# Kernel tuning notes

Measured on AMD Instinct MI355X. Metric: run time of the kernel, lower is better.

## Reference

```python
import jax, jax.numpy as jnp
import numpy as np

NUM_HEADS = 8
HEAD_DIM = 64  # inner_dim 512 / 8 heads
SCALE = HEAD_DIM ** -0.5


def setup_inputs() -> dict:
    key = jax.random.key(0)
    kq, kk, kv, kp = jax.random.split(key, 4)
    B, S, D = 8, 1024, 512
    q = jax.random.normal(kq, (B, S, D), dtype=jnp.float32)
    k = jax.random.normal(kk, (B, S, D), dtype=jnp.float32)
    v = jax.random.normal(kv, (B, S, D), dtype=jnp.float32)
    # learned additive positional bias table (trunc-normal init approximated by normal clipped)
    pos_bias = jnp.clip(jax.random.normal(kp, (1, NUM_HEADS, S, S), dtype=jnp.float32), -2.0, 2.0)
    return {"q": q, "k": k, "v": v, "pos_bias": pos_bias}


def reference(q, k, v, pos_bias):
    B, S, D = q.shape
    h, d = NUM_HEADS, HEAD_DIM
    # b n (h d) -> b h n d
    qh = q.reshape(B, S, h, d).transpose(0, 2, 1, 3) * SCALE
    kh = k.reshape(B, S, h, d).transpose(0, 2, 1, 3)
    vh = v.reshape(B, S, h, d).transpose(0, 2, 1, 3)
    sim = jnp.einsum('bhid,bhjd->bhij', qh, kh) + pos_bias
    attn = jax.nn.softmax(sim, axis=-1)
    out = jnp.einsum('bhij,bhjd->bhid', attn, vh)
    # b h n d -> b n (h d)
    return out.transpose(0, 2, 1, 3).reshape(B, S, h * d)
```

## Files before the change

### kernel.cpp

```cpp
#include <hip/hip_runtime.h>
#include <hip/hip_bf16.h>
#include <math.h>


typedef __attribute__((ext_vector_type(8))) short short8;
typedef __attribute__((ext_vector_type(4))) float f32x4;
typedef __attribute__((ext_vector_type(4))) unsigned short u16x4;

#define SEQ   1024
#define DM    512
#define HD    64
#define SCALE 0.125f

__device__ __forceinline__ unsigned short f2bf(float f) {
    unsigned u = __float_as_uint(f);
    u += 0x7fffu + ((u >> 16) & 1u);
    return (unsigned short)(u >> 16);
}

__device__ __forceinline__ u16x4 pack4(float a, float b, float c, float d) {
    u16x4 r; r[0] = f2bf(a); r[1] = f2bf(b); r[2] = f2bf(c); r[3] = f2bf(d);
    return r;
}

__global__ __launch_bounds__(256, 3)
void attn_fwd(const float* __restrict__ q, const float* __restrict__ k,
              const float* __restrict__ v, const float* __restrict__ bias,
              float* __restrict__ out)
{
    __shared__ short Klds[64][72];
    __shared__ short Vt[64][72];
    __shared__ short Plds[4][16][72];

    const int t    = threadIdx.x;
    const int wid  = t >> 6;
    const int lane = t & 63;
    const int qr   = lane & 15;
    const int g    = lane >> 4;

    int idx = blockIdx.x;
    const int b = idx & 7;  idx >>= 3;
    const int h = idx & 7;
    const int qtile = idx >> 3;
    const int qbase = qtile * 64 + wid * 16;

    const float* qp = q + ((b * SEQ + qbase + qr) * DM + h * HD);
    short8 qf[2];
#pragma unroll
    for (int c = 0; c < 2; ++c) {
        float4 x0 = *reinterpret_cast<const float4*>(qp + g * 8 + 32 * c);
        float4 x1 = *reinterpret_cast<const float4*>(qp + g * 8 + 32 * c + 4);
        short8 f;
        f[0] = (short)f2bf(x0.x * SCALE); f[1] = (short)f2bf(x0.y * SCALE);
        f[2] = (short)f2bf(x0.z * SCALE); f[3] = (short)f2bf(x0.w * SCALE);
        f[4] = (short)f2bf(x1.x * SCALE); f[5] = (short)f2bf(x1.y * SCALE);
        f[6] = (short)f2bf(x1.z * SCALE); f[7] = (short)f2bf(x1.w * SCALE);
        qf[c] = f;
    }

    f32x4 o[4];
#pragma unroll
    for (int nt = 0; nt < 4; ++nt) o[nt] = (f32x4){0.f, 0.f, 0.f, 0.f};
    float mrun = -INFINITY, lrun = 0.f;

    const int jrow = t & 63;
    const int cc   = t >> 6;

    for (int kt = 0; kt < 16; ++kt) {
        const int kbase = kt * 64;

        {
            const float4* kp4 = reinterpret_cast<const float4*>(
                k + ((b * SEQ + kbase + jrow) * DM + h * HD + cc * 16));
            float4 a0 = kp4[0], a1 = kp4[1], a2 = kp4[2], a3 = kp4[3];
            u16x4* dst = reinterpret_cast<u16x4*>(&Klds[jrow][cc * 16]);
            dst[0] = pack4(a0.x, a0.y, a0.z, a0.w);
            dst[1] = pack4(a1.x, a1.y, a1.z, a1.w);
            dst[2] = pack4(a2.x, a2.y, a2.z, a2.w);
            dst[3] = pack4(a3.x, a3.y, a3.z, a3.w);
        }
        {
            const float* vp = v + ((b * SEQ + kbase + cc * 16) * DM + h * HD + jrow);
            float vv[16];
#pragma unroll
            for (int jj = 0; jj < 16; ++jj) vv[jj] = vp[jj * DM];
            u16x4* dst = reinterpret_cast<u16x4*>(&Vt[jrow][cc * 16]);
            dst[0] = pack4(vv[0],  vv[1],  vv[2],  vv[3]);
            dst[1] = pack4(vv[4],  vv[5],  vv[6],  vv[7]);
            dst[2] = pack4(vv[8],  vv[9],  vv[10], vv[11]);
            dst[3] = pack4(vv[12], vv[13], vv[14], vv[15]);
        }
        __syncthreads();

        const float* bp = bias + ((h * SEQ + qbase + qr) * SEQ + kbase + g * 4);
        float4 bv0 = *reinterpret_cast<const float4*>(bp);
        float4 bv1 = *reinterpret_cast<const float4*>(bp + 16);
        float4 bv2 = *reinterpret_cast<const float4*>(bp + 32);
        float4 bv3 = *reinterpret_cast<const float4*>(bp + 48);

        f32x4 acc[4];
#pragma unroll
        for (int mt = 0; mt < 4; ++mt) {
            f32x4 a = (f32x4){0.f, 0.f, 0.f, 0.f};
#pragma unroll
            for (int c = 0; c < 2; ++c) {
                short8 kf = *reinterpret_cast<const short8*>(
                    &Klds[qr + 16 * mt][g * 8 + 32 * c]);
                a = __builtin_amdgcn_mfma_f32_16x16x32_bf16(kf, qf[c], a, 0, 0, 0);
            }
            acc[mt] = a;
        }
        acc[0][0] += bv0.x; acc[0][1] += bv0.y; acc[0][2] += bv0.z; acc[0][3] += bv0.w;
        acc[1][0] += bv1.x; acc[1][1] += bv1.y; acc[1][2] += bv1.z; acc[1][3] += bv1.w;
        acc[2][0] += bv2.x; acc[2][1] += bv2.y; acc[2][2] += bv2.z; acc[2][3] += bv2.w;
        acc[3][0] += bv3.x; acc[3][1] += bv3.y; acc[3][2] += bv3.z; acc[3][3] += bv3.w;

        float tmax = acc[0][0];
#pragma unroll
        for (int mt = 0; mt < 4; ++mt)
#pragma unroll
            for (int r = 0; r < 4; ++r) tmax = fmaxf(tmax, acc[mt][r]);
        tmax = fmaxf(tmax, __shfl_xor(tmax, 16));
        tmax = fmaxf(tmax, __shfl_xor(tmax, 32));
        const float mnew = fmaxf(mrun, tmax);

        float p[4][4];
        float ssum = 0.f;
#pragma unroll
        for (int mt = 0; mt < 4; ++mt)
#pragma unroll
            for (int r = 0; r < 4; ++r) {
                float e = __expf(acc[mt][r] - mnew);
                p[mt][r] = e;
                ssum += e;
            }
        ssum += __shfl_xor(ssum, 16);
        ssum += __shfl_xor(ssum, 32);
        const float sc = __expf(mrun - mnew);
        lrun = lrun * sc + ssum;
        mrun = mnew;

#pragma unroll
        for (int mt = 0; mt < 4; ++mt) {
            *reinterpret_cast<u16x4*>(&Plds[wid][qr][16 * mt + g * 4]) =
                pack4(p[mt][0], p[mt][1], p[mt][2], p[mt][3]);
        }

        float scr[4];
#pragma unroll
        for (int r = 0; r < 4; ++r) scr[r] = __shfl(sc, g * 4 + r);
#pragma unroll
        for (int nt = 0; nt < 4; ++nt)
#pragma unroll
            for (int r = 0; r < 4; ++r) o[nt][r] *= scr[r];

        asm volatile("s_waitcnt lgkmcnt(0)" ::: "memory");

        short8 pf0 = *reinterpret_cast<const short8*>(&Plds[wid][qr][g * 8]);
        short8 pf1 = *reinterpret_cast<const short8*>(&Plds[wid][qr][g * 8 + 32]);
#pragma unroll
        for (int nt = 0; nt < 4; ++nt) {
            short8 vf0 = *reinterpret_cast<const short8*>(&Vt[qr + 16 * nt][g * 8]);
            short8 vf1 = *reinterpret_cast<const short8*>(&Vt[qr + 16 * nt][g * 8 + 32]);
            o[nt] = __builtin_amdgcn_mfma_f32_16x16x32_bf16(pf0, vf0, o[nt], 0, 0, 0);
            o[nt] = __builtin_amdgcn_mfma_f32_16x16x32_bf16(pf1, vf1, o[nt], 0, 0, 0);
        }
        __syncthreads();
    }

    const float inv = 1.0f / lrun;
    float invr[4];
#pragma unroll
    for (int r = 0; r < 4; ++r) invr[r] = __shfl(inv, g * 4 + r);

    float* op = out + ((b * SEQ + qbase) * DM + h * HD + qr);
#pragma unroll
    for (int nt = 0; nt < 4; ++nt)
#pragma unroll
        for (int r = 0; r < 4; ++r)
            op[(g * 4 + r) * DM + nt * 16] = o[nt][r] * invr[r];
}

extern "C" void kernel_launch(void* const* d_in, const int* in_sizes, int n_in,
                              void* d_out, int out_size, void* d_ws, size_t ws_size,
                              hipStream_t stream) {
    const float* q    = (const float*)d_in[0];
    const float* k    = (const float*)d_in[1];
    const float* v    = (const float*)d_in[2];
    const float* bias = (const float*)d_in[3];
    float* out        = (float*)d_out;
    attn_fwd<<<dim3(8 * 8 * 16), dim3(256), 0, stream>>>(q, k, v, bias, out);
}
```

Baseline: 179.5 us.

## Pre-convert K/V to swizzled bf16 tiles and double-buffer them via LDS DMA

Two prep kernels convert K to bf16 and V to transposed bf16 in workspace, stored in 64x64 tiles with an XOR swizzle. The main kernel now handles 128 query rows per block, 32 per wave, so each K/V tile is reused across two 16-row subtiles. It loads tiles with global_load_lds double buffering, uses exp2 with log2e folded into the Q scale, and raises priority around the MFMA sections. This is meant to cut the redundant per-block fp32 K/V loads and conversions, including the strided transpose load of V, and to hide load latency. In exchange it adds two extra launches and a workspace round-trip, and halves the grid to 512 blocks.

```diff
diff --git a/kernel.cpp b/kernel.cpp
--- a/kernel.cpp
+++ b/kernel.cpp
@@ -10,17 +10,256 @@
 #define SEQ   1024
 #define DM    512
 #define HD    64
-#define SCALE 0.125f
+#define NH    8
+#define LOG2E 1.4426950408889634f
+#define QSCALE (0.125f * LOG2E)
 
 __device__ __forceinline__ unsigned short f2bf(float f) {
     unsigned u = __float_as_uint(f);
     u += 0x7fffu + ((u >> 16) & 1u);
     return (unsigned short)(u >> 16);
 }
-
 __device__ __forceinline__ u16x4 pack4(float a, float b, float c, float d) {
     u16x4 r; r[0] = f2bf(a); r[1] = f2bf(b); r[2] = f2bf(c); r[3] = f2bf(d);
     return r;
+}
+__device__ __forceinline__ short8 pack8(const float* x) {
+    short8 r;
+#pragma unroll
+    for (int i = 0; i < 8; ++i) r[i] = (short)f2bf(x[i]);
+    return r;
+}
+__device__ __forceinline__ float fexp2(float x) {
+#if __has_builtin(__builtin_amdgcn_exp2f)
+    return __builtin_amdgcn_exp2f(x);
+#else
+    return exp2f(x);
+#endif
+}
+__device__ __forceinline__ void gll16(const void* g, void* l) {
+    __builtin_amdgcn_global_load_lds(
+        (const __attribute__((address_space(1))) unsigned*)g,
+        (__attribute__((address_space(3))) unsigned*)l, 16, 0, 0);
+}
+
+__global__ __launch_bounds__(256)
+void prep_k(const float* __restrict__ k, short* __restrict__ kws) {
+    int tid = blockIdx.x * 256 + threadIdx.x;
+    int d8 = tid & 7, h = (tid >> 3) & 7, s = (tid >> 6) & 1023, b = tid >> 16;
+    const float* src = k + ((size_t)(b * SEQ + s) * DM + h * HD + d8 * 8);
+    float4 x0 = *(const float4*)src, x1 = *(const float4*)(src + 4);
+    float xs[8] = {x0.x, x0.y, x0.z, x0.w, x1.x, x1.y, x1.z, x1.w};
+    int bh = b * NH + h;
+    size_t idx = (size_t)(bh * 16 + (s >> 6)) * 4096 + (s & 63) * 64 + ((d8 ^ (s & 7)) * 8);
+    *(short8*)(kws + idx) = pack8(xs);
+}
+
+__global__ __launch_bounds__(256)
+void prep_v(const float* __restrict__ v, short* __restrict__ vtws) {
+    __shared__ short Vs[64][72];
+    int bid = blockIdx.x;
+    int st = bid & 15, h = (bid >> 4) & 7, b = bid >> 7;
+    int t = threadIdx.x;
+    {
+        int sl = t >> 2, dc = t & 3;
+        const float* src = v + ((size_t)(b * SEQ + st * 64 + sl) * DM + h * HD + dc * 16);
+        float4 a0 = ((const float4*)src)[0], a1 = ((const float4*)src)[1],
+               a2 = ((const float4*)src)[2], a3 = ((const float4*)src)[3];
+        float xs0[8] = {a0.x, a0.y, a0.z, a0.w, a1.x, a1.y, a1.z, a1.w};
+        float xs1[8] = {a2.x, a2.y, a2.z, a2.w, a3.x, a3.y, a3.z, a3.w};
+        *(short8*)&Vs[sl][dc * 16]     = pack8(xs0);
+        *(short8*)&Vs[sl][dc * 16 + 8] = pack8(xs1);
+    }
+    __syncthreads();
+    {
+        int d = t >> 2, sc = t & 3;
+        short vals[16];
+#pragma unroll
+        for (int j = 0; j < 16; ++j) vals[j] = Vs[sc * 16 + j][d];
+        short8 w0, w1;
+#pragma unroll
+        for (int j = 0; j < 8; ++j) { w0[j] = vals[j]; w1[j] = vals[8 + j]; }
+        int bh = b * NH + h;
+        size_t base = (size_t)(bh * 16 + st) * 4096 + d * 64;
+        int c0 = (sc * 2) ^ (d & 7), c1 = (sc * 2 + 1) ^ (d & 7);
+        *(short8*)(vtws + base + c0 * 8) = w0;
+        *(short8*)(vtws + base + c1 * 8) = w1;
+    }
+}
+
+__global__ __launch_bounds__(256, 2)
+void attn_fwd2(const float* __restrict__ q, const float* __restrict__ bias,
+               const short* __restrict__ kws, const short* __restrict__ vtws,
+               float* __restrict__ out)
+{
+    __shared__ short Ksh[2][4096];
+    __shared__ short Vsh[2][4096];
+    __shared__ short Plds[4][32][72];
+
+    const int t = threadIdx.x;
+    const int wid = t >> 6, lane = t & 63;
+    const int qr = lane & 15, g = lane >> 4;
+
+    int idx = blockIdx.x;
+    const int b = idx & 7;  idx >>= 3;
+    const int h = idx & 7;
+    const int qt = idx >> 3;
+    const int qbw = qt * 128 + wid * 32;
+    const int bh = b * NH + h;
+
+    short8 qf[2][2];
+#pragma unroll
+    for (int sub = 0; sub < 2; ++sub) {
+        const float* qp = q + ((size_t)(b * SEQ + qbw + sub * 16 + qr) * DM + h * HD);
+#pragma unroll
+        for (int c = 0; c < 2; ++c) {
+            float4 x0 = *(const float4*)(qp + g * 8 + 32 * c);
+            float4 x1 = *(const float4*)(qp + g * 8 + 32 * c + 4);
+            float xs[8] = {x0.x * QSCALE, x0.y * QSCALE, x0.z * QSCALE, x0.w * QSCALE,
+                           x1.x * QSCALE, x1.y * QSCALE, x1.z * QSCALE, x1.w * QSCALE};
+            qf[sub][c] = pack8(xs);
+        }
+    }
+
+    f32x4 o[2][4];
+#pragma unroll
+    for (int sub = 0; sub < 2; ++sub)
+#pragma unroll
+        for (int nt = 0; nt < 4; ++nt) o[sub][nt] = (f32x4){0.f, 0.f, 0.f, 0.f};
+    float m0 = -INFINITY, m1 = -INFINITY, l0 = 0.f, l1 = 0.f;
+
+    const size_t tb0 = (size_t)bh * 16 * 4096;
+    {
+        const short* gk = kws + tb0 + wid * 512 + lane * 8;
+        const short* gv = vtws + tb0 + wid * 512 + lane * 8;
+        gll16(gk,        &Ksh[0][wid * 512]);
+        gll16(gk + 2048, &Ksh[0][2048 + wid * 512]);
+        gll16(gv,        &Vsh[0][wid * 512]);
+        gll16(gv + 2048, &Vsh[0][2048 + wid * 512]);
+    }
+    __syncthreads();
+
+    int cur = 0;
+    for (int kt = 0; kt < 16; ++kt) {
+        if (kt < 15) {
+            const size_t tb = tb0 + (size_t)(kt + 1) * 4096;
+            const short* gk = kws + tb + wid * 512 + lane * 8;
+            const short* gv = vtws + tb + wid * 512 + lane * 8;
+            int nxt = cur ^ 1;
+            gll16(gk,        &Ksh[nxt][wid * 512]);
+            gll16(gk + 2048, &Ksh[nxt][2048 + wid * 512]);
+            gll16(gv,        &Vsh[nxt][wid * 512]);
+            gll16(gv + 2048, &Vsh[nxt][2048 + wid * 512]);
+        }
+
+        float4 bv[2][4];
+#pragma unroll
+        for (int sub = 0; sub < 2; ++sub) {
+            const float* bp = bias + ((size_t)(h * SEQ + qbw + sub * 16 + qr) * SEQ + kt * 64 + g * 4);
+#pragma unroll
+            for (int mt = 0; mt < 4; ++mt) bv[sub][mt] = *(const float4*)(bp + 16 * mt);
+        }
+
+        f32x4 acc[2][4];
+#pragma unroll
+        for (int sub = 0; sub < 2; ++sub)
+#pragma unroll
+            for (int mt = 0; mt < 4; ++mt) acc[sub][mt] = (f32x4){0.f, 0.f, 0.f, 0.f};
+        __builtin_amdgcn_s_setprio(1);
+#pragma unroll
+        for (int mt = 0; mt < 4; ++mt) {
+#pragma unroll
+            for (int c = 0; c < 2; ++c) {
+                const short8 kf = *(const short8*)
+                    &Ksh[cur][(qr + 16 * mt) * 64 + ((g + 4 * c) ^ (qr & 7)) * 8];
+                acc[0][mt] = __builtin_amdgcn_mfma_f32_16x16x32_bf16(kf, qf[0][c], acc[0][mt], 0, 0, 0);
+                acc[1][mt] = __builtin_amdgcn_mfma_f32_16x16x32_bf16(kf, qf[1][c], acc[1][mt], 0, 0, 0);
+            }
+        }
+        __builtin_amdgcn_s_setprio(0);
+
+        float sc[2];
+#pragma unroll
+        for (int sub = 0; sub < 2; ++sub) {
+            float s[4][4];
+            float tmax = -INFINITY;
+#pragma unroll
+            for (int mt = 0; mt < 4; ++mt)
+#pragma unroll
+                for (int r = 0; r < 4; ++r) {
+                    float val = fmaf(((const float*)&bv[sub][mt])[r], LOG2E, acc[sub][mt][r]);
+                    s[mt][r] = val;
+                    tmax = fmaxf(tmax, val);
+                }
+            tmax = fmaxf(tmax, __shfl_xor(tmax, 16));
+            tmax = fmaxf(tmax, __shfl_xor(tmax, 32));
+            const float mold = (sub == 0) ? m0 : m1;
+            const float mnew = fmaxf(mold, tmax);
+            float ssum = 0.f;
+#pragma unroll
+            for (int mt = 0; mt < 4; ++mt) {
+                float e0 = fexp2(s[mt][0] - mnew);
+                float e1 = fexp2(s[mt][1] - mnew);
+                float e2 = fexp2(s[mt][2] - mnew);
+                float e3 = fexp2(s[mt][3] - mnew);
+                ssum += (e0 + e1) + (e2 + e3);
+                *(u16x4*)&Plds[wid][sub * 16 + qr][16 * mt + g * 4] = pack4(e0, e1, e2, e3);
+            }
+            ssum += __shfl_xor(ssum, 16);
+            ssum += __shfl_xor(ssum, 32);
+            const float scs = fexp2(mold - mnew);
+            if (sub == 0) { l0 = l0 * scs + ssum; m0 = mnew; }
+            else          { l1 = l1 * scs + ssum; m1 = mnew; }
+            sc[sub] = scs;
+        }
+
+#pragma unroll
+        for (int sub = 0; sub < 2; ++sub) {
+            float scr[4];
+#pragma unroll
+            for (int r = 0; r < 4; ++r) scr[r] = __shfl(sc[sub], g * 4 + r);
+#pragma unroll
+            for (int nt = 0; nt < 4; ++nt)
+#pragma unroll
+                for (int r = 0; r < 4; ++r) o[sub][nt][r] *= scr[r];
+        }
+
+        asm volatile("s_waitcnt lgkmcnt(0)" ::: "memory");
+        __builtin_amdgcn_sched_barrier(0);
+
+        __builtin_amdgcn_s_setprio(1);
+#pragma unroll
+        for (int c = 0; c < 2; ++c) {
+            short8 pf0 = *(const short8*)&Plds[wid][qr][g * 8 + 32 * c];
+            short8 pf1 = *(const short8*)&Plds[wid][16 + qr][g * 8 + 32 * c];
+#pragma unroll
+            for (int nt = 0; nt < 4; ++nt) {
+                short8 vf = *(const short8*)
+                    &Vsh[cur][(qr + 16 * nt) * 64 + ((g + 4 * c) ^ (qr & 7)) * 8];
+                o[0][nt] = __builtin_amdgcn_mfma_f32_16x16x32_bf16(pf0, vf, o[0][nt], 0, 0, 0);
+                o[1][nt] = __builtin_amdgcn_mfma_f32_16x16x32_bf16(pf1, vf, o[1][nt], 0, 0, 0);
+            }
+        }
+        __builtin_amdgcn_s_setprio(0);
+
+        __syncthreads();
+        cur ^= 1;
+    }
+
+    const float inv0 = 1.0f / l0, inv1 = 1.0f / l1;
+#pragma unroll
+    for (int sub = 0; sub < 2; ++sub) {
+        const float invv = sub ? inv1 : inv0;
+        float invr[4];
+#pragma unroll
+        for (int r = 0; r < 4; ++r) invr[r] = __shfl(invv, g * 4 + r);
+        float* op = out + ((size_t)(b * SEQ + qbw + sub * 16) * DM + h * HD + qr);
+#pragma unroll
+        for (int nt = 0; nt < 4; ++nt)
+#pragma unroll
+            for (int r = 0; r < 4; ++r)
+                op[(size_t)(g * 4 + r) * DM + nt * 16] = o[sub][nt][r] * invr[r];
+    }
 }
 
 __global__ __launch_bounds__(256, 3)
@@ -30,13 +269,13 @@
 {
     __shared__ short Klds[64][72];
     __shared__ short Vt[64][72];
-    __shared__ short Plds[4][16][72];
-
-    const int t    = threadIdx.x;
-    const int wid  = t >> 6;
+    __shared__ short Pl[4][16][72];
+
+    const int t = threadIdx.x;
+    const int wid = t >> 6;
     const int lane = t & 63;
-    const int qr   = lane & 15;
-    const int g    = lane >> 4;
+    const int qr = lane & 15;
+    const int g = lane >> 4;
 
     int idx = blockIdx.x;
     const int b = idx & 7;  idx >>= 3;
@@ -50,12 +289,9 @@
     for (int c = 0; c < 2; ++c) {
         float4 x0 = *reinterpret_cast<const float4*>(qp + g * 8 + 32 * c);
         float4 x1 = *reinterpret_cast<const float4*>(qp + g * 8 + 32 * c + 4);
-        short8 f;
-        f[0] = (short)f2bf(x0.x * SCALE); f[1] = (short)f2bf(x0.y * SCALE);
-        f[2] = (short)f2bf(x0.z * SCALE); f[3] = (short)f2bf(x0.w * SCALE);
-        f[4] = (short)f2bf(x1.x * SCALE); f[5] = (short)f2bf(x1.y * SCALE);
-        f[6] = (short)f2bf(x1.z * SCALE); f[7] = (short)f2bf(x1.w * SCALE);
-        qf[c] = f;
+        float xs[8] = {x0.x * 0.125f, x0.y * 0.125f, x0.z * 0.125f, x0.w * 0.125f,
+                       x1.x * 0.125f, x1.y * 0.125f, x1.z * 0.125f, x1.w * 0.125f};
+        qf[c] = pack8(xs);
     }
 
     f32x4 o[4];
@@ -64,11 +300,10 @@
     float mrun = -INFINITY, lrun = 0.f;
 
     const int jrow = t & 63;
-    const int cc   = t >> 6;
+    const int cc = t >> 6;
 
     for (int kt = 0; kt < 16; ++kt) {
         const int kbase = kt * 64;
-
         {
             const float4* kp4 = reinterpret_cast<const float4*>(
                 k + ((b * SEQ + kbase + jrow) * DM + h * HD + cc * 16));
@@ -85,9 +320,9 @@
 #pragma unroll
             for (int jj = 0; jj < 16; ++jj) vv[jj] = vp[jj * DM];
             u16x4* dst = reinterpret_cast<u16x4*>(&Vt[jrow][cc * 16]);
-            dst[0] = pack4(vv[0],  vv[1],  vv[2],  vv[3]);
-            dst[1] = pack4(vv[4],  vv[5],  vv[6],  vv[7]);
-            dst[2] = pack4(vv[8],  vv[9],  vv[10], vv[11]);
+            dst[0] = pack4(vv[0], vv[1], vv[2], vv[3]);
+            dst[1] = pack4(vv[4], vv[5], vv[6], vv[7]);
+            dst[2] = pack4(vv[8], vv[9], vv[10], vv[11]);
             dst[3] = pack4(vv[12], vv[13], vv[14], vv[15]);
         }
         __syncthreads();
@@ -136,28 +371,29 @@
             }
         ssum += __shfl_xor(ssum, 16);
         ssum += __shfl_xor(ssum, 32);
-        const float sc = __expf(mrun - mnew);
-        lrun = lrun * sc + ssum;
+        const float scv = __expf(mrun - mnew);
+        lrun = lrun * scv + ssum;
         mrun = mnew;
 
 #pragma unroll
         for (int mt = 0; mt < 4; ++mt) {
-            *reinterpret_cast<u16x4*>(&Plds[wid][qr][16 * mt + g * 4]) =
+            *reinterpret_cast<u16x4*>(&Pl[wid][qr][16 * mt + g * 4]) =
                 pack4(p[mt][0], p[mt][1], p[mt][2], p[mt][3]);
         }
 
         float scr[4];
 #pragma unroll
-        for (int r = 0; r < 4; ++r) scr[r] = __shfl(sc, g * 4 + r);
+        for (int r = 0; r < 4; ++r) scr[r] = __shfl(scv, g * 4 + r);
 #pragma unroll
         for (int nt = 0; nt < 4; ++nt)
 #pragma unroll
             for (int r = 0; r < 4; ++r) o[nt][r] *= scr[r];
 
         asm volatile("s_waitcnt lgkmcnt(0)" ::: "memory");
-
-        short8 pf0 = *reinterpret_cast<const short8*>(&Plds[wid][qr][g * 8]);
-        short8 pf1 = *reinterpret_cast<const short8*>(&Plds[wid][qr][g * 8 + 32]);
+        __builtin_amdgcn_sched_barrier(0);
+
+        short8 pf0 = *reinterpret_cast<const short8*>(&Pl[wid][qr][g * 8]);
+        short8 pf1 = *reinterpret_cast<const short8*>(&Pl[wid][qr][g * 8 + 32]);
 #pragma unroll
         for (int nt = 0; nt < 4; ++nt) {
             short8 vf0 = *reinterpret_cast<const short8*>(&Vt[qr + 16 * nt][g * 8]);
@@ -189,5 +425,16 @@
     const float* v    = (const float*)d_in[2];
     const float* bias = (const float*)d_in[3];
     float* out        = (float*)d_out;
-    attn_fwd<<<dim3(8 * 8 * 16), dim3(256), 0, stream>>>(q, k, v, bias, out);
-}
+
+    const size_t elems = (size_t)8 * NH * SEQ * HD;
+    const size_t need  = 2 * elems * sizeof(short);
+    if (ws_size >= need) {
+        short* kws  = (short*)d_ws;
+        short* vtws = kws + elems;
+        prep_k<<<dim3(2048), dim3(256), 0, stream>>>(k, kws);
+        prep_v<<<dim3(1024), dim3(256), 0, stream>>>(v, vtws);
+        attn_fwd2<<<dim3(512), dim3(256), 0, stream>>>(q, bias, kws, vtws, out);
+    } else {
+        attn_fwd<<<dim3(1024), dim3(256), 0, stream>>>(q, k, v, bias, out);
+    }
+}
```

Result: faster. 161.5 us (-10.0%).
